# Optimization experiments

Hardware: AMD Instinct MI355X
Metric: run time of the kernel (lower is better)

## Reference

```python
import jax, jax.numpy as jnp
import numpy as np

D = 128          # embed_dim
V = 200000       # num_symbols (pad idx = V)
B = 4096         # query batch
BS = 1           # support batch (one-shot)
M = 50           # max neighbors
STEPS = 4        # process_steps
DM = 2 * D       # d_model = 256
H = 2 * DM       # LSTM hidden = 512
EPS = 1e-3       # LayerNormalization eps in source repo


def setup_inputs() -> dict:
    key = jax.random.key(0)
    ks = jax.random.split(key, 32)
    nrm = lambda k, s: jax.random.normal(k, s, jnp.float32) * 0.05
    ri = lambda k, s, hi: jax.random.randint(k, s, 0, hi)
    emb = nrm(ks[0], (V + 1, D)).at[V].set(0.0)  # padding_idx row zeroed
    return {
        "query": ri(ks[1], (B, 2), V),
        "support": ri(ks[2], (BS, 2), V),
        "q_l1": ri(ks[3], (B, M, 2), V + 1),
        "q_l2": ri(ks[4], (B, M, 2), V + 1),
        "q_deg_l": ri(ks[5], (B,), M),
        "q_r1": ri(ks[6], (B, M, 2), V + 1),
        "q_r2": ri(ks[7], (B, M, 2), V + 1),
        "q_deg_r": ri(ks[8], (B,), M),
        "s_l1": ri(ks[9], (BS, M, 2), V + 1),
        "s_l2": ri(ks[10], (BS, M, 2), V + 1),
        "s_deg_l": ri(ks[11], (BS,), M),
        "s_r1": ri(ks[12], (BS, M, 2), V + 1),
        "s_r2": ri(ks[13], (BS, M, 2), V + 1),
        "s_deg_r": ri(ks[14], (BS,), M),
        "emb": emb,
        "gcn_W": nrm(ks[15], (D, 2 * D)),
        "gcn_lb": jnp.zeros(D, jnp.float32),   # nn.Linear bias of gcn_w
        "gcn_b": jnp.zeros(D, jnp.float32),    # extra gcn_b parameter
        "attn_W": nrm(ks[16], (1, D)),
        "attn_b": jnp.zeros(1, jnp.float32),
        "gate_W": nrm(ks[17], (1, D)),
        "gate_lb": jnp.zeros(1, jnp.float32),   # nn.Linear bias of gate_w
        "gate_b": jnp.zeros(1, jnp.float32),    # extra gate_b parameter
        "p1_W": nrm(ks[18], (2 * DM, DM)),
        "p1_b": jnp.zeros(2 * DM, jnp.float32),
        "p2_W": nrm(ks[19], (DM, 2 * DM)),
        "p2_b": jnp.zeros(DM, jnp.float32),
        "ln_a": jnp.ones(DM, jnp.float32),
        "ln_b": jnp.zeros(DM, jnp.float32),
        "Wih": nrm(ks[20], (4 * H, DM)),
        "Whh": nrm(ks[21], (4 * H, H)),
        "bih": jnp.zeros(4 * H, jnp.float32),
        "bhh": jnp.zeros(4 * H, jnp.float32),
    }


def reference(query, support, q_l1, q_l2, q_deg_l, q_r1, q_r2, q_deg_r,
              s_l1, s_l2, s_deg_l, s_r1, s_r2, s_deg_r,
              emb, gcn_W, gcn_lb, gcn_b, attn_W, attn_b,
              gate_W, gate_lb, gate_b, p1_W, p1_b, p2_W, p2_b,
              ln_a, ln_b, Wih, Whh, bih, bhh):
    # dropout is identity (eval / p=0). deg tensors are unused, as in source.

    def nbr(conn, self_ids):
        # conn: [b, M, 2] -> gather rel/ent embeddings, project, attend, gate
        rel = emb[conn[:, :, 0]]            # [b, M, D]
        ent = emb[conn[:, :, 1]]            # [b, M, D]
        x = jnp.concatenate([rel, ent], axis=-1)             # [b, M, 2D]
        proj = jnp.einsum('bmc,dc->bmd', x, gcn_W) + gcn_lb + gcn_b
        proj = jnp.where(proj >= 0, proj, 0.01 * proj)        # leaky_relu
        scores = jnp.einsum('bmd,od->bmo', proj, attn_W) + attn_b  # [b, M, 1]
        w = jax.nn.softmax(scores, axis=1)
        agg = jnp.sum(proj * w, axis=1)                       # [b, D]
        gate = jax.nn.sigmoid(agg @ gate_W.T + gate_lb + gate_b)  # [b, 1]
        return gate * agg + (1.0 - gate) * emb[self_ids]

    def pair_vec(h_ids, t_ids, l1, l2, r1, r2):
        left = (nbr(l1, h_ids) + nbr(l2, h_ids)) / 2.0
        right = (nbr(r1, t_ids) + nbr(r2, t_ids)) / 2.0
        return jnp.concatenate([left, right], axis=-1)        # [b, 2D]

    qv = pair_vec(query[:, 0], query[:, 1], q_l1, q_l2, q_r1, q_r2)   # [B, DM]
    sv = pair_vec(support[:, 0], support[:, 1], s_l1, s_l2, s_r1, s_r2)  # [BS, DM]

    # SupportEncoder: FFN + residual + LayerNormalization (std w/ Bessel, eps=1e-3)
    h = jax.nn.relu(sv @ p1_W.T + p1_b) @ p2_W.T + p2_b + sv
    mu = h.mean(-1, keepdims=True)
    sig = jnp.std(h, axis=-1, keepdims=True, ddof=1)
    sg = (h - mu) / (sig + EPS) * ln_a + ln_b                 # [BS, DM]

    # QueryEncoder: process-attention LSTM (torch LSTMCell gate order i,f,g,o)
    def step(carry, _):
        hq, h_r, c = carry
        g = qv @ Wih.T + bih + h_r @ Whh.T + bhh
        i, f, gg, o = jnp.split(g, 4, axis=-1)
        c = jax.nn.sigmoid(f) * c + jax.nn.sigmoid(i) * jnp.tanh(gg)
        hh = jax.nn.sigmoid(o) * jnp.tanh(c)
        hq = qv + hh[:, :DM]
        a = jax.nn.softmax(hq @ sg.T, axis=1)                 # [B, BS]
        r = a @ sg                                            # [B, DM]
        return (hq, jnp.concatenate([hq, r], axis=1), c), None

    z = jnp.zeros((qv.shape[0], H), qv.dtype)
    (qg, _, _), _ = jax.lax.scan(step, (qv, z, z), None, length=STEPS)

    return jnp.sum(qg * sg, axis=1)                           # [B]
```

## Files before the change

kernel.cpp:

```cpp
#include <hip/hip_runtime.h>

#define D    128
#define VSZ  200000
#define NB   4096
#define MM   50
#define DM   256
#define HSZ  512
#define G4   2048

typedef __attribute__((ext_vector_type(8))) short short8;
typedef __attribute__((ext_vector_type(4))) float floatx4;

__device__ __forceinline__ float sigf(float x) { return 1.0f / (1.0f + __expf(-x)); }
__device__ __forceinline__ float tanhfast(float x) { return 1.0f - 2.0f / (__expf(2.0f * x) + 1.0f); }
__device__ __forceinline__ unsigned short f2bf(float x) {
    unsigned int u = __float_as_uint(x);
    u += 0x7FFFu + ((u >> 16) & 1u);
    return (unsigned short)(u >> 16);
}
__device__ __forceinline__ float bf2f(unsigned short s) {
    return __uint_as_float(((unsigned int)s) << 16);
}

__device__ __forceinline__ void async_copy16(void* lds, const void* gsrc) {
    __builtin_amdgcn_global_load_lds(
        (const __attribute__((address_space(1))) unsigned int*)gsrc,
        (__attribute__((address_space(3))) unsigned int*)lds, 16, 0, 0);
}

__global__ __launch_bounds__(256) void k_wconv(
    const float* __restrict__ gcn_W, unsigned short* __restrict__ Wb)
{
    int i = blockIdx.x * 256 + threadIdx.x;
    int n = i >> 7, k = i & 127;
    float v = (n < 128) ? gcn_W[n * 256 + k] : gcn_W[(n - 128) * 256 + 128 + k];
    Wb[i] = f2bf(v);
}

__global__ __launch_bounds__(256) void k_pack(
    const float* __restrict__ Wih, const float* __restrict__ Whh,
    const float* __restrict__ bih, const float* __restrict__ bhh,
    unsigned short* __restrict__ Wihp, unsigned short* __restrict__ Whhp,
    float* __restrict__ gb)
{
    int idx = blockIdx.x * 256 + threadIdx.x;
    if (idx < 131072) {
        int ci = idx & 65535;
        int lane = ci & 63, rest = ci >> 6;
        int ks = rest & 7, tile = rest >> 3;
        int n = tile * 16 + (lane & 15), k = ks * 32 + (lane >> 4) * 8;
        const float* src = (idx < 65536) ? (Wih + (size_t)n * 256 + k)
                                         : (Whh + (size_t)n * 512 + k);
        unsigned short* dst = (idx < 65536) ? Wihp : Whhp;
        short8 o;
        #pragma unroll
        for (int j = 0; j < 8; ++j) o[j] = (short)f2bf(src[j]);
        *(short8*)(dst + (size_t)ci * 8) = o;
    } else if (idx < 131072 + 2048) {
        int i = idx - 131072;
        gb[i] = bih[i] + bhh[i];
    }
}

__global__ __launch_bounds__(256, 4) void k_proj_mfma(
    const float* __restrict__ emb, const unsigned short* __restrict__ Wb,
    const float* __restrict__ gcn_lb, const float* __restrict__ gcn_b,
    unsigned short* __restrict__ P1, unsigned short* __restrict__ P2, int nrows)
{
    __shared__ unsigned short S[16896];
    int t = threadIdx.x;
    int v0 = blockIdx.x * 64;
    int lane = t & 63, w = t >> 6;
    int nl = lane & 15, quad = lane >> 4;
    int n0 = w * 64;

    #pragma unroll
    for (int it = 0; it < 8; ++it) {
        int chunk = w * 8 + it;
        int o = chunk * 1024 + lane * 16;
        int row = o >> 9;
        int b = o & 511;
        int bs = b ^ ((row & 7) << 5);
        int v = v0 + row;
        v = (v < nrows) ? v : (nrows - 1);
        async_copy16((char*)S + chunk * 1024,
                     (const char*)emb + (size_t)v * 512 + bs);
    }
    __syncthreads();

    floatx4 acc[4][4];
    #pragma unroll
    for (int mt = 0; mt < 4; ++mt)
        #pragma unroll
        for (int nt = 0; nt < 4; ++nt)
            acc[mt][nt] = (floatx4){0.f, 0.f, 0.f, 0.f};

    const char* Sb = (const char*)S;
    #pragma unroll
    for (int ks = 0; ks < 4; ++ks) {
        short8 bfr[4];
        #pragma unroll
        for (int nt = 0; nt < 4; ++nt)
            bfr[nt] = *(const short8*)(Wb + (size_t)(n0 + nt * 16 + nl) * 128 + ks * 32 + quad * 8);
        short8 af[4];
        #pragma unroll
        for (int mt = 0; mt < 4; ++mt) {
            int row = mt * 16 + nl;
            int b = ks * 128 + quad * 32;
            int ba = row * 512 + (b ^ ((row & 7) << 5));
            float4 lo = *(const float4*)(Sb + ba);
            float4 hi = *(const float4*)(Sb + ba + 16);
            short8 a;
            a[0] = (short)f2bf(lo.x); a[1] = (short)f2bf(lo.y);
            a[2] = (short)f2bf(lo.z); a[3] = (short)f2bf(lo.w);
            a[4] = (short)f2bf(hi.x); a[5] = (short)f2bf(hi.y);
            a[6] = (short)f2bf(hi.z); a[7] = (short)f2bf(hi.w);
            af[mt] = a;
        }
        #pragma unroll
        for (int mt = 0; mt < 4; ++mt)
            #pragma unroll
            for (int nt = 0; nt < 4; ++nt)
                acc[mt][nt] = __builtin_amdgcn_mfma_f32_16x16x32_bf16(
                    af[mt], bfr[nt], acc[mt][nt], 0, 0, 0);
    }

    __syncthreads();
    #pragma unroll
    for (int nt = 0; nt < 4; ++nt) {
        int col = n0 + nt * 16 + nl;
        float bias = (col < 128) ? (gcn_lb[col] + gcn_b[col]) : 0.f;
        #pragma unroll
        for (int mt = 0; mt < 4; ++mt)
            #pragma unroll
            for (int reg = 0; reg < 4; ++reg)
                S[(mt * 16 + quad * 4 + reg) * 264 + col] =
                    f2bf(acc[mt][nt][reg] + bias);
    }
    __syncthreads();
    #pragma unroll
    for (int it = 0; it < 8; ++it) {
        int c = t + 256 * it;
        int row = c >> 5, c8 = c & 31;
        int v = v0 + row;
        if (v < nrows) {
            int4 val = *(const int4*)(S + row * 264 + c8 * 8);
            unsigned short* dst = (c8 < 16) ? (P1 + (size_t)v * D + c8 * 8)
                                            : (P2 + (size_t)v * D + (c8 - 16) * 8);
            *(int4*)dst = val;
        }
    }
}

__global__ __launch_bounds__(256) void k_nbr(
    const int* __restrict__ query, const int* __restrict__ support,
    const int* __restrict__ q_l1, const int* __restrict__ q_l2,
    const int* __restrict__ q_r1, const int* __restrict__ q_r2,
    const int* __restrict__ s_l1, const int* __restrict__ s_l2,
    const int* __restrict__ s_r1, const int* __restrict__ s_r2,
    const unsigned short* __restrict__ P1, const unsigned short* __restrict__ P2,
    const float* __restrict__ emb,
    const float* __restrict__ attn_W, const float* __restrict__ attn_b,
    const float* __restrict__ gate_W, const float* __restrict__ gate_lb,
    const float* __restrict__ gate_b,
    float* __restrict__ qv, unsigned short* __restrict__ qvbf,
    float* __restrict__ sv)
{
    __shared__ unsigned short proj[2 * MM * 136];
    __shared__ int rel[2 * MM], ent[2 * MM];
    __shared__ float scw[2 * 64];
    __shared__ float scp[2][2][64];
    __shared__ float aw[D], gw[D];
    __shared__ float redg[4];
    __shared__ float gateS[2];
    __shared__ float oth[D];

    int bid = blockIdx.x;
    int item = bid >> 1;
    int side = bid & 1;
    int t = threadIdx.x;

    const int* cA; const int* cB; int selfid; float* outp; bool isq;
    if (item < NB) {
        isq = true;
        cA = (side ? q_r1 : q_l1) + (size_t)item * MM * 2;
        cB = (side ? q_r2 : q_l2) + (size_t)item * MM * 2;
        selfid = query[item * 2 + side];
        outp = qv + (size_t)item * DM + side * D;
    } else {
        isq = false;
        int i2 = item - NB;
        cA = (side ? s_r1 : s_l1) + (size_t)i2 * MM * 2;
        cB = (side ? s_r2 : s_l2) + (size_t)i2 * MM * 2;
        selfid = support[i2 * 2 + side];
        outp = sv + (size_t)i2 * DM + side * D;
    }
    if (t < D) { aw[t] = attn_W[t]; gw[t] = gate_W[t]; }
    if (t < 2 * MM) {
        const int* c = (t < MM) ? cA : cB;
        int m = (t < MM) ? t : t - MM;
        rel[t] = c[m * 2]; ent[t] = c[m * 2 + 1];
    }
    __syncthreads();
    for (int e8 = t; e8 < 2 * MM * 16; e8 += 256) {
        int m = e8 >> 4, d8 = (e8 & 15) * 8;
        short8 a = *(const short8*)(P1 + (size_t)rel[m] * D + d8);
        short8 b = *(const short8*)(P2 + (size_t)ent[m] * D + d8);
        short8 o;
        #pragma unroll
        for (int j = 0; j < 8; ++j) {
            float p = bf2f((unsigned short)a[j]) + bf2f((unsigned short)b[j]);
            p = (p >= 0.f) ? p : 0.01f * p;
            o[j] = (short)f2bf(p);
        }
        *(short8*)(proj + m * 136 + d8) = o;
    }
    __syncthreads();
    {
        int tab = t >> 7, g = (t >> 6) & 1, m = t & 63;
        float s = 0.f;
        if (m < MM) {
            const unsigned short* pr = proj + (tab * MM + m) * 136 + g * 64;
            #pragma unroll
            for (int i = 0; i < 8; ++i) {
                short8 v8 = *(const short8*)(pr + i * 8);
                #pragma unroll
                for (int j = 0; j < 8; ++j)
                    s += bf2f((unsigned short)v8[j]) * aw[g * 64 + i * 8 + j];
            }
        }
        scp[tab][g][m] = s;
    }
    __syncthreads();
    if (t < 128) {
        int tab = t >> 6, m = t & 63;
        float v = (m < MM) ? (scp[tab][0][m] + scp[tab][1][m] + attn_b[0]) : -1e30f;
        float mx = v;
        #pragma unroll
        for (int o = 32; o > 0; o >>= 1) mx = fmaxf(mx, __shfl_xor(mx, o, 64));
        float ev = (m < MM) ? __expf(v - mx) : 0.f;
        float sm = ev;
        #pragma unroll
        for (int o = 32; o > 0; o >>= 1) sm += __shfl_xor(sm, o, 64);
        if (m < MM) scw[tab * 64 + m] = ev / sm;
    }
    __syncthreads();
    int tab = t >> 7, d = t & 127;
    float agg = 0.f;
    #pragma unroll 5
    for (int m = 0; m < MM; ++m)
        agg += scw[tab * 64 + m] * bf2f(proj[(tab * MM + m) * 136 + d]);
    float gpart = agg * gw[d];
    #pragma unroll
    for (int o = 32; o > 0; o >>= 1) gpart += __shfl_xor(gpart, o, 64);
    if ((t & 63) == 0) redg[t >> 6] = gpart;
    __syncthreads();
    if (t == 0)  gateS[0] = sigf(redg[0] + redg[1] + gate_lb[0] + gate_b[0]);
    if (t == 64) gateS[1] = sigf(redg[2] + redg[3] + gate_lb[0] + gate_b[0]);
    __syncthreads();
    float embd = emb[(size_t)selfid * D + d];
    float val = gateS[tab] * agg + (1.f - gateS[tab]) * embd;
    if (tab == 1) oth[d] = val;
    __syncthreads();
    if (tab == 0) {
        float r = 0.5f * (val + oth[d]);
        outp[d] = r;
        if (isq) qvbf[(size_t)item * DM + side * D + d] = f2bf(r);
    }
}

__global__ __launch_bounds__(256) void k_sg1(
    const float* __restrict__ sv, const float* __restrict__ p1_W,
    const float* __restrict__ p1_b, float* __restrict__ hid)
{
    __shared__ float s[DM];
    int t = threadIdx.x;
    s[t] = sv[t];
    __syncthreads();
    int j = blockIdx.x * 32 + (t >> 3);
    int pp = t & 7;
    const float* w = p1_W + (size_t)j * DM + pp * 32;
    float a = 0.f;
    #pragma unroll
    for (int i = 0; i < 8; ++i) {
        float4 v = *(const float4*)(w + i * 4);
        int c = pp * 32 + i * 4;
        a += v.x * s[c] + v.y * s[c + 1] + v.z * s[c + 2] + v.w * s[c + 3];
    }
    a += __shfl_xor(a, 1, 64);
    a += __shfl_xor(a, 2, 64);
    a += __shfl_xor(a, 4, 64);
    if (pp == 0) hid[j] = fmaxf(a + p1_b[j], 0.f);
}

__global__ __launch_bounds__(256) void k_sg2(
    const float* __restrict__ sv, const float* __restrict__ hid,
    const float* __restrict__ p2_W, const float* __restrict__ p2_b,
    float* __restrict__ h)
{
    __shared__ float hs[2 * DM];
    int t = threadIdx.x;
    hs[t] = hid[t]; hs[t + 256] = hid[t + 256];
    __syncthreads();
    int r = blockIdx.x * 32 + (t >> 3);
    int pp = t & 7;
    const float* w = p2_W + (size_t)r * (2 * DM) + pp * 64;
    float a = 0.f;
    #pragma unroll
    for (int i = 0; i < 16; ++i) {
        float4 v = *(const float4*)(w + i * 4);
        int c = pp * 64 + i * 4;
        a += v.x * hs[c] + v.y * hs[c + 1] + v.z * hs[c + 2] + v.w * hs[c + 3];
    }
    a += __shfl_xor(a, 1, 64);
    a += __shfl_xor(a, 2, 64);
    a += __shfl_xor(a, 4, 64);
    if (pp == 0) h[r] = a + p2_b[r] + sv[r];
}

__global__ __launch_bounds__(256) void k_sg3(
    const float* __restrict__ h, const float* __restrict__ ln_a,
    const float* __restrict__ ln_b, float* __restrict__ sg)
{
    __shared__ float red[8];
    int t = threadIdx.x;
    float x = h[t];
    float sm = x;
    #pragma unroll
    for (int o = 32; o > 0; o >>= 1) sm += __shfl_xor(sm, o, 64);
    if ((t & 63) == 0) red[t >> 6] = sm;
    __syncthreads();
    float mu = (red[0] + red[1] + red[2] + red[3]) * (1.0f / 256.0f);
    float dv = x - mu;
    float sq = dv * dv;
    #pragma unroll
    for (int o = 32; o > 0; o >>= 1) sq += __shfl_xor(sq, o, 64);
    if ((t & 63) == 0) red[4 + (t >> 6)] = sq;
    __syncthreads();
    float var = (red[4] + red[5] + red[6] + red[7]) * (1.0f / 255.0f);
    float sig = sqrtf(var);
    sg[t] = dv / (sig + 0.001f) * ln_a[t] + ln_b[t];
}

__global__ __launch_bounds__(256) void k_sgwhh(
    const float* __restrict__ sg, const float* __restrict__ Whh,
    float* __restrict__ sgW)
{
    __shared__ float s[DM];
    int t = threadIdx.x;
    s[t] = sg[t];
    __syncthreads();
    int k = blockIdx.x * 64 + (t >> 2);
    int pp = t & 3;
    const float* w = Whh + (size_t)k * HSZ + DM + pp * 64;
    float a = 0.f;
    #pragma unroll
    for (int i = 0; i < 16; ++i) {
        float4 v = *(const float4*)(w + i * 4);
        int c = pp * 64 + i * 4;
        a += v.x * s[c] + v.y * s[c + 1] + v.z * s[c + 2] + v.w * s[c + 3];
    }
    a += __shfl_xor(a, 1, 64);
    a += __shfl_xor(a, 2, 64);
    if (pp == 0) sgW[k] = a;
}

__global__ __launch_bounds__(256) void k_zero(float* __restrict__ p)
{
    p[blockIdx.x * 256 + threadIdx.x] = 0.f;
}

__global__ __launch_bounds__(256, 4) void k_lstm(
    const float* __restrict__ qv, const unsigned short* __restrict__ Ain,
    const unsigned short* __restrict__ Bp,
    const float* __restrict__ gb, const float* __restrict__ sgW,
    const unsigned short* __restrict__ g0i, unsigned short* __restrict__ g0o,
    float4* __restrict__ Cf, unsigned short* __restrict__ hqo,
    const float* __restrict__ sg, float* __restrict__ out, int mode)
{
    int t = threadIdx.x;
    int lane = t & 63, w = t >> 6;
    int nl = lane & 15, quad = lane >> 4;
    int bx = blockIdx.x;
    int b0 = bx * 32;
    int T = blockIdx.y * 4 + w;

    floatx4 acc[2][4];
    #pragma unroll
    for (int mt = 0; mt < 2; ++mt)
        #pragma unroll
        for (int g = 0; g < 4; ++g) acc[mt][g] = (floatx4){0.f, 0.f, 0.f, 0.f};

    for (int ks = 0; ks < 8; ++ks) {
        short8 af0 = *(const short8*)(Ain + (size_t)(b0 + nl) * DM + ks * 32 + quad * 8);
        short8 af1 = *(const short8*)(Ain + (size_t)(b0 + 16 + nl) * DM + ks * 32 + quad * 8);
        #pragma unroll
        for (int g = 0; g < 4; ++g) {
            short8 bfr = *(const short8*)(Bp + ((size_t)((T + 32 * g) * 8 + ks) * 64 + lane) * 8);
            acc[0][g] = __builtin_amdgcn_mfma_f32_16x16x32_bf16(af0, bfr, acc[0][g], 0, 0, 0);
            acc[1][g] = __builtin_amdgcn_mfma_f32_16x16x32_bf16(af1, bfr, acc[1][g], 0, 0, 0);
        }
    }

    int coli = T * 16 + nl;
    float preg[2][4] = {{0.f, 0.f, 0.f, 0.f}, {0.f, 0.f, 0.f, 0.f}};
    #pragma unroll
    for (int mt = 0; mt < 2; ++mt) {
        size_t cfi = (((size_t)bx * 32 + T) * 2 + mt) * 64 + lane;
        if (mode == 0) {
            float bi = gb[coli], bff = gb[coli + 512];
            float bg = gb[coli + 1024], bo = gb[coli + 1536];
            float4 cn4; ushort4 pk[4];
            #pragma unroll
            for (int r = 0; r < 4; ++r) {
                float gi_ = acc[mt][0][r] + bi;
                float gf_ = acc[mt][1][r] + bff;
                float gg_ = acc[mt][2][r] + bg;
                float go_ = acc[mt][3][r] + bo;
                float cn = sigf(gi_) * tanhfast(gg_);
                (&cn4.x)[r] = cn;
                ((unsigned short*)&pk[0])[r] = f2bf(gi_);
                ((unsigned short*)&pk[1])[r] = f2bf(gf_);
                ((unsigned short*)&pk[2])[r] = f2bf(gg_);
                ((unsigned short*)&pk[3])[r] = f2bf(go_);
                if (T < 16) {
                    int b = b0 + mt * 16 + quad * 4 + r;
                    float h = qv[(size_t)b * DM + coli] + sigf(go_) * tanhfast(cn);
                    hqo[(size_t)b * DM + coli] = f2bf(h);
                }
            }
            #pragma unroll
            for (int g = 0; g < 4; ++g) {
                size_t gfi = ((((size_t)bx * 128 + g * 32 + T) * 2 + mt) * 64 + lane) * 4;
                *(ushort4*)(g0o + gfi) = pk[g];
            }
            Cf[cfi] = cn4;
        } else {
            float si = sgW[coli], sf = sgW[coli + 512];
            float sgg = sgW[coli + 1024], so = sgW[coli + 1536];
            ushort4 gld[4];
            #pragma unroll
            for (int g = 0; g < 4; ++g) {
                size_t gfi = ((((size_t)bx * 128 + g * 32 + T) * 2 + mt) * 64 + lane) * 4;
                gld[g] = *(const ushort4*)(g0i + gfi);
            }
            float4 cold = Cf[cfi];
            float4 cn4;
            #pragma unroll
            for (int r = 0; r < 4; ++r) {
                float gi_ = acc[mt][0][r] + si  + bf2f(((unsigned short*)&gld[0])[r]);
                float gf_ = acc[mt][1][r] + sf  + bf2f(((unsigned short*)&gld[1])[r]);
                float gg_ = acc[mt][2][r] + sgg + bf2f(((unsigned short*)&gld[2])[r]);
                float go_ = acc[mt][3][r] + so  + bf2f(((unsigned short*)&gld[3])[r]);
                float cn = sigf(gf_) * (&cold.x)[r] + sigf(gi_) * tanhfast(gg_);
                (&cn4.x)[r] = cn;
                if (T < 16) {
                    int b = b0 + mt * 16 + quad * 4 + r;
                    float h = qv[(size_t)b * DM + coli] + sigf(go_) * tanhfast(cn);
                    if (mode == 1) hqo[(size_t)b * DM + coli] = f2bf(h);
                    else           preg[mt][r] += h * sg[coli];
                }
            }
            if (mode == 1) Cf[cfi] = cn4;
        }
    }

    if (mode == 2) {
        #pragma unroll
        for (int mt = 0; mt < 2; ++mt)
            #pragma unroll
            for (int r = 0; r < 4; ++r) {
                float p = preg[mt][r];
                p += __shfl_xor(p, 1, 64);
                p += __shfl_xor(p, 2, 64);
                p += __shfl_xor(p, 4, 64);
                p += __shfl_xor(p, 8, 64);
                if (nl == 0)
                    atomicAdd(out + b0 + mt * 16 + quad * 4 + r, p);
            }
    }
}

extern "C" void kernel_launch(void* const* d_in, const int* in_sizes, int n_in,
                              void* d_out, int out_size, void* d_ws, size_t ws_size,
                              hipStream_t stream) {
    const int* query   = (const int*)d_in[0];
    const int* support = (const int*)d_in[1];
    const int* q_l1 = (const int*)d_in[2];
    const int* q_l2 = (const int*)d_in[3];
    const int* q_r1 = (const int*)d_in[5];
    const int* q_r2 = (const int*)d_in[6];
    const int* s_l1 = (const int*)d_in[8];
    const int* s_l2 = (const int*)d_in[9];
    const int* s_r1 = (const int*)d_in[11];
    const int* s_r2 = (const int*)d_in[12];
    const float* emb    = (const float*)d_in[14];
    const float* gcn_W  = (const float*)d_in[15];
    const float* gcn_lb = (const float*)d_in[16];
    const float* gcn_b  = (const float*)d_in[17];
    const float* attn_W = (const float*)d_in[18];
    const float* attn_b = (const float*)d_in[19];
    const float* gate_W = (const float*)d_in[20];
    const float* gate_lb = (const float*)d_in[21];
    const float* gate_b  = (const float*)d_in[22];
    const float* p1_W = (const float*)d_in[23];
    const float* p1_b = (const float*)d_in[24];
    const float* p2_W = (const float*)d_in[25];
    const float* p2_b = (const float*)d_in[26];
    const float* ln_a = (const float*)d_in[27];
    const float* ln_b = (const float*)d_in[28];
    const float* Wih  = (const float*)d_in[29];
    const float* Whh  = (const float*)d_in[30];
    const float* bih  = (const float*)d_in[31];
    const float* bhh  = (const float*)d_in[32];

    unsigned short* P1   = (unsigned short*)d_ws;
    unsigned short* P2   = P1 + (size_t)(VSZ + 1) * D;
    unsigned short* Wb   = P2 + (size_t)(VSZ + 1) * D;
    unsigned short* Wihp = Wb + 256 * 128;
    unsigned short* Whhp = Wihp + (size_t)65536 * 8;
    unsigned short* g0b  = Whhp + (size_t)65536 * 8;
    unsigned short* hqA  = g0b + (size_t)NB * G4;
    unsigned short* hqB  = hqA + (size_t)NB * DM;
    unsigned short* qvbf = hqB + (size_t)NB * DM;
    float* fws = (float*)(qvbf + (size_t)NB * DM);
    float* gbv = fws;  fws += G4;
    float* qvb = fws;  fws += (size_t)NB * DM;
    float* svb = fws;  fws += DM;
    float* sgb = fws;  fws += DM;
    float* sgW = fws;  fws += G4 + 4;
    float* hidb = fws; fws += 2 * DM;
    float* hb  = fws;  fws += DM;
    float4* Cf = (float4*)fws;  fws += (size_t)NB * HSZ;
    (void)in_sizes; (void)n_in; (void)out_size; (void)ws_size;

    k_wconv<<<128, 256, 0, stream>>>(gcn_W, Wb);
    k_pack<<<(131072 + 2048) / 256, 256, 0, stream>>>(
        Wih, Whh, bih, bhh, Wihp, Whhp, gbv);
    k_proj_mfma<<<(VSZ + 1 + 63) / 64, 256, 0, stream>>>(
        emb, Wb, gcn_lb, gcn_b, P1, P2, VSZ + 1);
    k_nbr<<<2 * (NB + 1), 256, 0, stream>>>(
        query, support, q_l1, q_l2, q_r1, q_r2, s_l1, s_l2, s_r1, s_r2,
        P1, P2, emb, attn_W, attn_b, gate_W, gate_lb, gate_b, qvb, qvbf, svb);
    k_sg1<<<16, 256, 0, stream>>>(svb, p1_W, p1_b, hidb);
    k_sg2<<<8, 256, 0, stream>>>(svb, hidb, p2_W, p2_b, hb);
    k_sg3<<<1, 256, 0, stream>>>(hb, ln_a, ln_b, sgb);
    k_sgwhh<<<32, 256, 0, stream>>>(sgb, Whh, sgW);
    k_lstm<<<dim3(NB / 32, 8), 256, 0, stream>>>(
        qvb, qvbf, Wihp, gbv, sgW, g0b, g0b, Cf, hqA, sgb, (float*)d_out, 0);
    k_lstm<<<dim3(NB / 32, 8), 256, 0, stream>>>(
        qvb, hqA, Whhp, gbv, sgW, g0b, g0b, Cf, hqB, sgb, (float*)d_out, 1);
    k_lstm<<<dim3(NB / 32, 8), 256, 0, stream>>>(
        qvb, hqB, Whhp, gbv, sgW, g0b, g0b, Cf, hqA, sgb, (float*)d_out, 1);
    k_zero<<<NB / 256, 256, 0, stream>>>((float*)d_out);
    k_lstm<<<dim3(NB / 32, 4), 256, 0, stream>>>(
        qvb, hqA, Whhp, gbv, sgW, g0b, g0b, Cf, hqB, sgb, (float*)d_out, 2);
}
```

Before: 419.1 us.

## Fuse four LSTM step kernels into one persistent-per-batch-tile kernel

Replaces the four separate LSTM step launches (plus the output zeroing kernel) with one kernel where each 512-thread block owns 16 query rows for all steps. Hidden state moves through LDS and cell state and gate pre-activations stay in registers, removing the global round-trips for g0, C and hq. The final dot product is reduced in LDS and written directly instead of with atomics. The weight-conversion kernel is also merged into the packing kernel to save a launch. The trade-off is only 256 blocks, each streaming the full packed weights every step, so occupancy and L2 weight traffic may limit it.

```diff
diff --git a/kernel.cpp b/kernel.cpp
--- a/kernel.cpp
+++ b/kernel.cpp
@@ -28,20 +28,12 @@
         (__attribute__((address_space(3))) unsigned int*)lds, 16, 0, 0);
 }
 
-__global__ __launch_bounds__(256) void k_wconv(
-    const float* __restrict__ gcn_W, unsigned short* __restrict__ Wb)
-{
-    int i = blockIdx.x * 256 + threadIdx.x;
-    int n = i >> 7, k = i & 127;
-    float v = (n < 128) ? gcn_W[n * 256 + k] : gcn_W[(n - 128) * 256 + 128 + k];
-    Wb[i] = f2bf(v);
-}
-
 __global__ __launch_bounds__(256) void k_pack(
     const float* __restrict__ Wih, const float* __restrict__ Whh,
     const float* __restrict__ bih, const float* __restrict__ bhh,
+    const float* __restrict__ gcn_W,
     unsigned short* __restrict__ Wihp, unsigned short* __restrict__ Whhp,
-    float* __restrict__ gb)
+    float* __restrict__ gb, unsigned short* __restrict__ Wb)
 {
     int idx = blockIdx.x * 256 + threadIdx.x;
     if (idx < 131072) {
@@ -59,6 +51,11 @@
     } else if (idx < 131072 + 2048) {
         int i = idx - 131072;
         gb[i] = bih[i] + bhh[i];
+    } else if (idx < 131072 + 2048 + 32768) {
+        int i = idx - (131072 + 2048);
+        int n = i >> 7, k = i & 127;
+        float v = (n < 128) ? gcn_W[n * 256 + k] : gcn_W[(n - 128) * 256 + 128 + k];
+        Wb[i] = f2bf(v);
     }
 }
 
@@ -365,119 +362,164 @@
     if (pp == 0) sgW[k] = a;
 }
 
-__global__ __launch_bounds__(256) void k_zero(float* __restrict__ p)
-{
-    p[blockIdx.x * 256 + threadIdx.x] = 0.f;
-}
-
-__global__ __launch_bounds__(256, 4) void k_lstm(
-    const float* __restrict__ qv, const unsigned short* __restrict__ Ain,
-    const unsigned short* __restrict__ Bp,
+__global__ __launch_bounds__(512, 2) void k_lstm_fused(
+    const float* __restrict__ qv, const unsigned short* __restrict__ qvbf,
+    const unsigned short* __restrict__ Wihp, const unsigned short* __restrict__ Whhp,
     const float* __restrict__ gb, const float* __restrict__ sgW,
-    const unsigned short* __restrict__ g0i, unsigned short* __restrict__ g0o,
-    float4* __restrict__ Cf, unsigned short* __restrict__ hqo,
-    const float* __restrict__ sg, float* __restrict__ out, int mode)
-{
+    const float* __restrict__ sg, float* __restrict__ out)
+{
+    __shared__ unsigned short Ab[16 * 264];
+    __shared__ float redbuf[8][16];
     int t = threadIdx.x;
     int lane = t & 63, w = t >> 6;
     int nl = lane & 15, quad = lane >> 4;
-    int bx = blockIdx.x;
-    int b0 = bx * 32;
-    int T = blockIdx.y * 4 + w;
-
-    floatx4 acc[2][4];
-    #pragma unroll
-    for (int mt = 0; mt < 2; ++mt)
-        #pragma unroll
-        for (int g = 0; g < 4; ++g) acc[mt][g] = (floatx4){0.f, 0.f, 0.f, 0.f};
-
-    for (int ks = 0; ks < 8; ++ks) {
-        short8 af0 = *(const short8*)(Ain + (size_t)(b0 + nl) * DM + ks * 32 + quad * 8);
-        short8 af1 = *(const short8*)(Ain + (size_t)(b0 + 16 + nl) * DM + ks * 32 + quad * 8);
-        #pragma unroll
-        for (int g = 0; g < 4; ++g) {
-            short8 bfr = *(const short8*)(Bp + ((size_t)((T + 32 * g) * 8 + ks) * 64 + lane) * 8);
-            acc[0][g] = __builtin_amdgcn_mfma_f32_16x16x32_bf16(af0, bfr, acc[0][g], 0, 0, 0);
-            acc[1][g] = __builtin_amdgcn_mfma_f32_16x16x32_bf16(af1, bfr, acc[1][g], 0, 0, 0);
-        }
-    }
-
-    int coli = T * 16 + nl;
-    float preg[2][4] = {{0.f, 0.f, 0.f, 0.f}, {0.f, 0.f, 0.f, 0.f}};
-    #pragma unroll
-    for (int mt = 0; mt < 2; ++mt) {
-        size_t cfi = (((size_t)bx * 32 + T) * 2 + mt) * 64 + lane;
-        if (mode == 0) {
-            float bi = gb[coli], bff = gb[coli + 512];
-            float bg = gb[coli + 1024], bo = gb[coli + 1536];
-            float4 cn4; ushort4 pk[4];
-            #pragma unroll
-            for (int r = 0; r < 4; ++r) {
-                float gi_ = acc[mt][0][r] + bi;
-                float gf_ = acc[mt][1][r] + bff;
-                float gg_ = acc[mt][2][r] + bg;
-                float go_ = acc[mt][3][r] + bo;
-                float cn = sigf(gi_) * tanhfast(gg_);
-                (&cn4.x)[r] = cn;
-                ((unsigned short*)&pk[0])[r] = f2bf(gi_);
-                ((unsigned short*)&pk[1])[r] = f2bf(gf_);
-                ((unsigned short*)&pk[2])[r] = f2bf(gg_);
-                ((unsigned short*)&pk[3])[r] = f2bf(go_);
-                if (T < 16) {
-                    int b = b0 + mt * 16 + quad * 4 + r;
-                    float h = qv[(size_t)b * DM + coli] + sigf(go_) * tanhfast(cn);
-                    hqo[(size_t)b * DM + coli] = f2bf(h);
+    int b0 = blockIdx.x * 16;
+
+    {
+        int row = t >> 5, c16 = t & 31;
+        *(int4*)(Ab + row * 264 + c16 * 8) =
+            *(const int4*)(qvbf + (size_t)(b0 + row) * DM + c16 * 8);
+    }
+    int kt[2] = { w, w + 8 };
+
+    float sgWreg[2][4], qvreg[2][4], sgreg2[2];
+    float cc[2][4];
+    ushort4 g0s[2][4];
+    #pragma unroll
+    for (int j = 0; j < 2; ++j) {
+        #pragma unroll
+        for (int g = 0; g < 4; ++g)
+            sgWreg[j][g] = sgW[g * 512 + kt[j] * 16 + nl];
+        sgreg2[j] = sg[kt[j] * 16 + nl];
+        #pragma unroll
+        for (int r = 0; r < 4; ++r)
+            qvreg[j][r] = qv[(size_t)(b0 + quad * 4 + r) * DM + kt[j] * 16 + nl];
+    }
+    __syncthreads();
+
+    #pragma unroll 1
+    for (int st = 0; st < 3; ++st) {
+        short8 af[8];
+        #pragma unroll
+        for (int ks = 0; ks < 8; ++ks)
+            af[ks] = *(const short8*)(Ab + nl * 264 + ks * 32 + quad * 8);
+        const unsigned short* Bp = (st == 0) ? Wihp : Whhp;
+        floatx4 acc[2][4];
+        #pragma unroll
+        for (int j = 0; j < 2; ++j)
+            #pragma unroll
+            for (int g = 0; g < 4; ++g)
+                acc[j][g] = (floatx4){0.f, 0.f, 0.f, 0.f};
+        #pragma unroll
+        for (int j = 0; j < 2; ++j)
+            #pragma unroll
+            for (int g = 0; g < 4; ++g) {
+                int T = g * 32 + kt[j];
+                #pragma unroll
+                for (int ks = 0; ks < 8; ++ks) {
+                    short8 bfr = *(const short8*)(Bp + ((size_t)(T * 8 + ks) * 64 + lane) * 8);
+                    acc[j][g] = __builtin_amdgcn_mfma_f32_16x16x32_bf16(
+                        af[ks], bfr, acc[j][g], 0, 0, 0);
                 }
             }
-            #pragma unroll
-            for (int g = 0; g < 4; ++g) {
-                size_t gfi = ((((size_t)bx * 128 + g * 32 + T) * 2 + mt) * 64 + lane) * 4;
-                *(ushort4*)(g0o + gfi) = pk[g];
-            }
-            Cf[cfi] = cn4;
-        } else {
-            float si = sgW[coli], sf = sgW[coli + 512];
-            float sgg = sgW[coli + 1024], so = sgW[coli + 1536];
-            ushort4 gld[4];
-            #pragma unroll
-            for (int g = 0; g < 4; ++g) {
-                size_t gfi = ((((size_t)bx * 128 + g * 32 + T) * 2 + mt) * 64 + lane) * 4;
-                gld[g] = *(const ushort4*)(g0i + gfi);
-            }
-            float4 cold = Cf[cfi];
-            float4 cn4;
-            #pragma unroll
-            for (int r = 0; r < 4; ++r) {
-                float gi_ = acc[mt][0][r] + si  + bf2f(((unsigned short*)&gld[0])[r]);
-                float gf_ = acc[mt][1][r] + sf  + bf2f(((unsigned short*)&gld[1])[r]);
-                float gg_ = acc[mt][2][r] + sgg + bf2f(((unsigned short*)&gld[2])[r]);
-                float go_ = acc[mt][3][r] + so  + bf2f(((unsigned short*)&gld[3])[r]);
-                float cn = sigf(gf_) * (&cold.x)[r] + sigf(gi_) * tanhfast(gg_);
-                (&cn4.x)[r] = cn;
-                if (T < 16) {
-                    int b = b0 + mt * 16 + quad * 4 + r;
-                    float h = qv[(size_t)b * DM + coli] + sigf(go_) * tanhfast(cn);
-                    if (mode == 1) hqo[(size_t)b * DM + coli] = f2bf(h);
-                    else           preg[mt][r] += h * sg[coli];
+        float hval[2][4];
+        if (st == 0) {
+            #pragma unroll
+            for (int j = 0; j < 2; ++j) {
+                float bi  = gb[0 * 512 + kt[j] * 16 + nl];
+                float bf_ = gb[1 * 512 + kt[j] * 16 + nl];
+                float bg  = gb[2 * 512 + kt[j] * 16 + nl];
+                float bo  = gb[3 * 512 + kt[j] * 16 + nl];
+                #pragma unroll
+                for (int r = 0; r < 4; ++r) {
+                    float gi_ = acc[j][0][r] + bi;
+                    float gf_ = acc[j][1][r] + bf_;
+                    float gg_ = acc[j][2][r] + bg;
+                    float go_ = acc[j][3][r] + bo;
+                    ((unsigned short*)&g0s[j][0])[r] = f2bf(gi_);
+                    ((unsigned short*)&g0s[j][1])[r] = f2bf(gf_);
+                    ((unsigned short*)&g0s[j][2])[r] = f2bf(gg_);
+                    ((unsigned short*)&g0s[j][3])[r] = f2bf(go_);
+                    float cn = sigf(gi_) * tanhfast(gg_);
+                    cc[j][r] = cn;
+                    hval[j][r] = qvreg[j][r] + sigf(go_) * tanhfast(cn);
                 }
             }
-            if (mode == 1) Cf[cfi] = cn4;
+        } else {
+            #pragma unroll
+            for (int j = 0; j < 2; ++j)
+                #pragma unroll
+                for (int r = 0; r < 4; ++r) {
+                    float gi_ = acc[j][0][r] + sgWreg[j][0] + bf2f(((unsigned short*)&g0s[j][0])[r]);
+                    float gf_ = acc[j][1][r] + sgWreg[j][1] + bf2f(((unsigned short*)&g0s[j][1])[r]);
+                    float gg_ = acc[j][2][r] + sgWreg[j][2] + bf2f(((unsigned short*)&g0s[j][2])[r]);
+                    float go_ = acc[j][3][r] + sgWreg[j][3] + bf2f(((unsigned short*)&g0s[j][3])[r]);
+                    float cn = sigf(gf_) * cc[j][r] + sigf(gi_) * tanhfast(gg_);
+                    cc[j][r] = cn;
+                    hval[j][r] = qvreg[j][r] + sigf(go_) * tanhfast(cn);
+                }
         }
-    }
-
-    if (mode == 2) {
-        #pragma unroll
-        for (int mt = 0; mt < 2; ++mt)
+        __syncthreads();
+        #pragma unroll
+        for (int j = 0; j < 2; ++j)
+            #pragma unroll
+            for (int r = 0; r < 4; ++r)
+                Ab[(quad * 4 + r) * 264 + kt[j] * 16 + nl] = f2bf(hval[j][r]);
+        __syncthreads();
+    }
+
+    {
+        short8 af[8];
+        #pragma unroll
+        for (int ks = 0; ks < 8; ++ks)
+            af[ks] = *(const short8*)(Ab + nl * 264 + ks * 32 + quad * 8);
+        floatx4 acc[2][4];
+        #pragma unroll
+        for (int j = 0; j < 2; ++j)
+            #pragma unroll
+            for (int g = 0; g < 4; ++g)
+                acc[j][g] = (floatx4){0.f, 0.f, 0.f, 0.f};
+        #pragma unroll
+        for (int j = 0; j < 2; ++j)
+            #pragma unroll
+            for (int g = 0; g < 4; ++g) {
+                int T = g * 32 + kt[j];
+                #pragma unroll
+                for (int ks = 0; ks < 8; ++ks) {
+                    short8 bfr = *(const short8*)(Whhp + ((size_t)(T * 8 + ks) * 64 + lane) * 8);
+                    acc[j][g] = __builtin_amdgcn_mfma_f32_16x16x32_bf16(
+                        af[ks], bfr, acc[j][g], 0, 0, 0);
+                }
+            }
+        float part[4] = {0.f, 0.f, 0.f, 0.f};
+        #pragma unroll
+        for (int j = 0; j < 2; ++j)
             #pragma unroll
             for (int r = 0; r < 4; ++r) {
-                float p = preg[mt][r];
-                p += __shfl_xor(p, 1, 64);
-                p += __shfl_xor(p, 2, 64);
-                p += __shfl_xor(p, 4, 64);
-                p += __shfl_xor(p, 8, 64);
-                if (nl == 0)
-                    atomicAdd(out + b0 + mt * 16 + quad * 4 + r, p);
+                float gi_ = acc[j][0][r] + sgWreg[j][0] + bf2f(((unsigned short*)&g0s[j][0])[r]);
+                float gf_ = acc[j][1][r] + sgWreg[j][1] + bf2f(((unsigned short*)&g0s[j][1])[r]);
+                float gg_ = acc[j][2][r] + sgWreg[j][2] + bf2f(((unsigned short*)&g0s[j][2])[r]);
+                float go_ = acc[j][3][r] + sgWreg[j][3] + bf2f(((unsigned short*)&g0s[j][3])[r]);
+                float cn = sigf(gf_) * cc[j][r] + sigf(gi_) * tanhfast(gg_);
+                float h = qvreg[j][r] + sigf(go_) * tanhfast(cn);
+                part[r] += h * sgreg2[j];
             }
+        #pragma unroll
+        for (int r = 0; r < 4; ++r) {
+            float p = part[r];
+            p += __shfl_xor(p, 1, 64);
+            p += __shfl_xor(p, 2, 64);
+            p += __shfl_xor(p, 4, 64);
+            p += __shfl_xor(p, 8, 64);
+            if (nl == 0) redbuf[w][quad * 4 + r] = p;
+        }
+    }
+    __syncthreads();
+    if (t < 16) {
+        float s = 0.f;
+        #pragma unroll
+        for (int w2 = 0; w2 < 8; ++w2) s += redbuf[w2][t];
+        out[b0 + t] = s;
     }
 }
 
@@ -519,10 +561,7 @@
     unsigned short* Wb   = P2 + (size_t)(VSZ + 1) * D;
     unsigned short* Wihp = Wb + 256 * 128;
     unsigned short* Whhp = Wihp + (size_t)65536 * 8;
-    unsigned short* g0b  = Whhp + (size_t)65536 * 8;
-    unsigned short* hqA  = g0b + (size_t)NB * G4;
-    unsigned short* hqB  = hqA + (size_t)NB * DM;
-    unsigned short* qvbf = hqB + (size_t)NB * DM;
+    unsigned short* qvbf = Whhp + (size_t)65536 * 8;
     float* fws = (float*)(qvbf + (size_t)NB * DM);
     float* gbv = fws;  fws += G4;
     float* qvb = fws;  fws += (size_t)NB * DM;
@@ -531,12 +570,10 @@
     float* sgW = fws;  fws += G4 + 4;
     float* hidb = fws; fws += 2 * DM;
     float* hb  = fws;  fws += DM;
-    float4* Cf = (float4*)fws;  fws += (size_t)NB * HSZ;
     (void)in_sizes; (void)n_in; (void)out_size; (void)ws_size;
 
-    k_wconv<<<128, 256, 0, stream>>>(gcn_W, Wb);
-    k_pack<<<(131072 + 2048) / 256, 256, 0, stream>>>(
-        Wih, Whh, bih, bhh, Wihp, Whhp, gbv);
+    k_pack<<<648, 256, 0, stream>>>(
+        Wih, Whh, bih, bhh, gcn_W, Wihp, Whhp, gbv, Wb);
     k_proj_mfma<<<(VSZ + 1 + 63) / 64, 256, 0, stream>>>(
         emb, Wb, gcn_lb, gcn_b, P1, P2, VSZ + 1);
     k_nbr<<<2 * (NB + 1), 256, 0, stream>>>(
@@ -546,13 +583,6 @@
     k_sg2<<<8, 256, 0, stream>>>(svb, hidb, p2_W, p2_b, hb);
     k_sg3<<<1, 256, 0, stream>>>(hb, ln_a, ln_b, sgb);
     k_sgwhh<<<32, 256, 0, stream>>>(sgb, Whh, sgW);
-    k_lstm<<<dim3(NB / 32, 8), 256, 0, stream>>>(
-        qvb, qvbf, Wihp, gbv, sgW, g0b, g0b, Cf, hqA, sgb, (float*)d_out, 0);
-    k_lstm<<<dim3(NB / 32, 8), 256, 0, stream>>>(
-        qvb, hqA, Whhp, gbv, sgW, g0b, g0b, Cf, hqB, sgb, (float*)d_out, 1);
-    k_lstm<<<dim3(NB / 32, 8), 256, 0, stream>>>(
-        qvb, hqB, Whhp, gbv, sgW, g0b, g0b, Cf, hqA, sgb, (float*)d_out, 1);
-    k_zero<<<NB / 256, 256, 0, stream>>>((float*)d_out);
-    k_lstm<<<dim3(NB / 32, 4), 256, 0, stream>>>(
-        qvb, hqA, Whhp, gbv, sgW, g0b, g0b, Cf, hqB, sgb, (float*)d_out, 2);
-}
+    k_lstm_fused<<<256, 512, 0, stream>>>(
+        qvb, qvbf, Wihp, Whhp, gbv, sgW, sgb, (float*)d_out);
+}
```

New measurement: 378.5 us. 9.7% less time.
